# Optimization experiments

Measured on AMD Instinct MI355X. Metric: run time of the kernel, lower is better.

## Reference

```python
import jax, jax.numpy as jnp
import numpy as np

SIG_DEPTH = 4  # matches sig_depth init arg


def _outer(a, b):
    # flattened tensor product: [B, m] x [B, n] -> [B, m*n] (row-major, matches signatory layout)
    return (a[:, :, None] * b[:, None, :]).reshape(a.shape[0], -1)


def setup_inputs() -> dict:
    key = jax.random.key(0)
    k1, k2 = jax.random.split(key)
    B, L, Cin = 64, 256, 7
    out_dim = 512
    C = Cin + 1
    sig_channels = sum(C ** k for k in range(1, SIG_DEPTH + 1))  # 4680
    inp = jax.random.normal(k1, (B, L, Cin), dtype=jnp.float32)
    W = jax.random.normal(k2, (out_dim, sig_channels), dtype=jnp.float32) * 0.02
    b = jnp.zeros((out_dim,), dtype=jnp.float32)
    return {"inp": inp, "W": W, "b": b}


def reference(inp, W, b):
    B, L, Cin = inp.shape
    # Augment: prepend time channel linspace(0, 1, L), keep original channels
    t = jnp.broadcast_to(jnp.linspace(0.0, 1.0, L, dtype=inp.dtype)[None, :, None], (B, L, 1))
    x = jnp.concatenate([t, inp], axis=-1)  # [B, L, C]
    C = Cin + 1
    d = SIG_DEPTH
    dx = jnp.transpose(x[:, 1:] - x[:, :-1], (1, 0, 2))  # [L-1, B, C] increments
    init = tuple(jnp.zeros((B, C ** (k + 1)), x.dtype) for k in range(d))  # identity signature (all zero levels)

    def step(levels, v):
        # exp(v) in the truncated tensor algebra: e_k = v^{(x)k} / k!
        e = [v]
        for k in range(1, d):
            e.append(_outer(e[-1], v) / (k + 1))
        # Chen's identity: new_k = a_k + e_k + sum_{i=1}^{k-1} a_i (x) e_{k-i}
        new = []
        for k in range(d):
            acc = levels[k] + e[k]
            for i in range(k):
                acc = acc + _outer(levels[i], e[k - 1 - i])
            new.append(acc)
        sig = jnp.concatenate(new, axis=-1)  # [B, sig_channels]
        return tuple(new), sig

    _, sigs = jax.lax.scan(step, init, dx)  # [L-1, B, sig_channels] (stream=True)
    sigs = jnp.transpose(sigs, (1, 0, 2))   # [B, L-1, sig_channels]
    return sigs @ W.T + b                   # [B, L-1, out_dim]
```

## Files before the change

### kernel.cpp

```cpp
#include <hip/hip_runtime.h>
#include <hip/hip_bf16.h>

#define BATCH 64
#define LSEQ 256
#define CIN 7
#define CC 8
#define NSIG 4680
#define KPAD 4736
#define TSTEPS 255
#define ODIM 512
#define NCHUNK 16
#define CH 16
#define NKT 74
#define BM 256
#define BN 128

typedef __attribute__((ext_vector_type(8))) unsigned short ushort8;
typedef __attribute__((ext_vector_type(8))) __bf16 bf16x8;
typedef __attribute__((ext_vector_type(4))) float f32x4;

__device__ __forceinline__ unsigned short f2bf(float x) {
    __hip_bfloat16 h = __float2bfloat16(x);
    return *(unsigned short*)&h;
}

#define GLDS16(gp, lp)                                                      \
    __builtin_amdgcn_global_load_lds(                                       \
        (const __attribute__((address_space(1))) void*)(gp),                \
        (__attribute__((address_space(3))) void*)(lp), 16, 0, 0)

__global__ __launch_bounds__(512) void sig_ckpt_kernel(const float* __restrict__ inp,
                                                       float* __restrict__ ckpt) {
    __shared__ float sDx[TSTEPS * CC];

    const int b   = blockIdx.x;
    const int tid = threadIdx.x;

    const float* ip = inp + (size_t)b * LSEQ * CIN;
    for (int i = tid; i < TSTEPS * CC; i += 512) {
        int t = i >> 3, c = i & 7;
        sDx[i] = (c == 0) ? (1.0f / 255.0f)
                          : ip[(t + 1) * CIN + (c - 1)] - ip[t * CIN + (c - 1)];
    }
    __syncthreads();

    const int i1 = tid >> 6;
    const int i2 = (tid >> 3) & 7;
    const int i3 = tid & 7;

    float a1own = 0.0f, a2own = 0.0f, a3 = 0.0f;
    float a4[8];
#pragma unroll
    for (int e = 0; e < 8; ++e) a4[e] = 0.0f;

    for (int t = 0; t < 240; ++t) {
        const float* v = &sDx[t * CC];
        const float4 vlo = *(const float4*)&v[0];
        const float4 vhi = *(const float4*)&v[4];
        const float va = v[i1], vb = v[i2], vc = v[i3];
        const float e3s = va * vb * vc * (1.0f / 6.0f);
        const float T4 = e3s * 0.25f + a1own * vb * vc * (1.0f / 6.0f)
                       + a2own * vc * 0.5f + a3;
        a4[0] += vlo.x * T4; a4[1] += vlo.y * T4;
        a4[2] += vlo.z * T4; a4[3] += vlo.w * T4;
        a4[4] += vhi.x * T4; a4[5] += vhi.y * T4;
        a4[6] += vhi.z * T4; a4[7] += vhi.w * T4;
        a3 += e3s + (a1own * vb * 0.5f + a2own) * vc;
        a2own += vb * (0.5f * va + a1own);
        a1own += va;

        if (((t + 1) & 15) == 0) {
            const int c = ((t + 1) >> 4) - 1;
            float* cp = ckpt + ((size_t)b * 15 + c) * NSIG;
            if ((tid & 63) == 0) cp[i1] = a1own;
            if ((tid & 7) == 0) cp[8 + (tid >> 3)] = a2own;
            cp[72 + tid] = a3;
            float4 q0 = {a4[0], a4[1], a4[2], a4[3]};
            float4 q1 = {a4[4], a4[5], a4[6], a4[7]};
            *(float4*)&cp[584 + tid * 8]     = q0;
            *(float4*)&cp[584 + tid * 8 + 4] = q1;
        }
    }
}

__global__ __launch_bounds__(512) void sig_write_kernel(const float* __restrict__ inp,
                                                        const float* __restrict__ ckpt,
                                                        unsigned short* __restrict__ sig) {
    __shared__ float sDx[CH * CC];

    const int chunk = blockIdx.x;
    const int b     = blockIdx.y;
    const int tid   = threadIdx.x;
    const int t0    = chunk * CH;
    const int t1    = (chunk == NCHUNK - 1) ? TSTEPS : t0 + CH;

    const float* ip = inp + (size_t)b * LSEQ * CIN;
    for (int i = tid; i < (t1 - t0) * CC; i += 512) {
        int t = t0 + (i >> 3), c = i & 7;
        sDx[i] = (c == 0) ? (1.0f / 255.0f)
                          : ip[(t + 1) * CIN + (c - 1)] - ip[t * CIN + (c - 1)];
    }
    __syncthreads();

    const int i1 = tid >> 6;
    const int i2 = (tid >> 3) & 7;
    const int i3 = tid & 7;

    float a1own, a2own, a3;
    float a4[8];
    if (chunk == 0) {
        a1own = a2own = a3 = 0.0f;
#pragma unroll
        for (int e = 0; e < 8; ++e) a4[e] = 0.0f;
    } else {
        const float* cp = ckpt + ((size_t)b * 15 + (chunk - 1)) * NSIG;
        a1own = cp[i1];
        a2own = cp[8 + (tid >> 3)];
        a3    = cp[72 + tid];
        float4 q0 = *(const float4*)&cp[584 + tid * 8];
        float4 q1 = *(const float4*)&cp[584 + tid * 8 + 4];
        a4[0] = q0.x; a4[1] = q0.y; a4[2] = q0.z; a4[3] = q0.w;
        a4[4] = q1.x; a4[5] = q1.y; a4[6] = q1.z; a4[7] = q1.w;
    }

    for (int t = t0; t < t1; ++t) {
        const float* v = &sDx[(t - t0) * CC];
        const float4 vlo = *(const float4*)&v[0];
        const float4 vhi = *(const float4*)&v[4];
        const float va = v[i1], vb = v[i2], vc = v[i3];
        const float e3s = va * vb * vc * (1.0f / 6.0f);
        const float T4 = e3s * 0.25f + a1own * vb * vc * (1.0f / 6.0f)
                       + a2own * vc * 0.5f + a3;
        a4[0] += vlo.x * T4; a4[1] += vlo.y * T4;
        a4[2] += vlo.z * T4; a4[3] += vlo.w * T4;
        a4[4] += vhi.x * T4; a4[5] += vhi.y * T4;
        a4[6] += vhi.z * T4; a4[7] += vhi.w * T4;
        a3 += e3s + (a1own * vb * 0.5f + a2own) * vc;
        a2own += vb * (0.5f * va + a1own);
        a1own += va;

        unsigned short* row = sig + ((size_t)b * TSTEPS + t) * KPAD;
        ushort8 pack;
#pragma unroll
        for (int e = 0; e < 8; ++e) pack[e] = f2bf(a4[e]);
        *(ushort8*)(row + 584 + tid * 8) = pack;
        row[72 + tid] = f2bf(a3);
        if ((tid & 63) == 0) row[i1] = f2bf(a1own);
        if ((tid & 7) == 0) row[8 + (tid >> 3)] = f2bf(a2own);
        if (tid >= 448 && tid < 504) row[4232 + tid] = 0;
    }
}

__global__ __launch_bounds__(256) void wcvt_kernel(const float* __restrict__ W,
                                                   unsigned short* __restrict__ Wb) {
    int idx = blockIdx.x * 256 + threadIdx.x;
    if (idx >= ODIM * KPAD) return;
    int n = idx / KPAD, k = idx - n * KPAD;
    Wb[idx] = (k < NSIG) ? f2bf(W[(size_t)n * NSIG + k]) : (unsigned short)0;
}

__global__ __launch_bounds__(512) void gemm_kernel(const unsigned short* __restrict__ A,
                                                   const unsigned short* __restrict__ Wb,
                                                   const float* __restrict__ bias,
                                                   float* __restrict__ out,
                                                   int Mrows) {
    __shared__ unsigned short As[3][BM * 64];
    __shared__ unsigned short Bs[3][BN * 64];

    const int tid = threadIdx.x;
    int nt, mt;
    if (gridDim.y == 64) {
        const int li = blockIdx.y * 4 + blockIdx.x;
        const int x  = li & 7;
        const int j  = li >> 3;
        mt = x * 8 + (j >> 2);
        nt = j & 3;
    } else {
        nt = blockIdx.x; mt = blockIdx.y;
    }
    const int lane = tid & 63;
    const int wv   = tid >> 6;
    const int wr   = wv >> 1;
    const int wc   = wv & 1;
    const int lr   = lane & 15;
    const int lq   = lane >> 4;
    const int sb   = lr & 7;

    const f32x4 z4 = {0.0f, 0.0f, 0.0f, 0.0f};
    f32x4 acc[4][4];
#pragma unroll
    for (int i = 0; i < 4; ++i)
#pragma unroll
        for (int j = 0; j < 4; ++j) acc[i][j] = z4;

    const int srow = tid >> 3;
    const int gcb  = (tid & 7) ^ (srow & 7);
    const int scol = gcb * 8;

    const unsigned short* aptr[4];
    const unsigned short* bptr[2];
#pragma unroll
    for (int i = 0; i < 4; ++i) {
        int gr = mt * BM + i * 64 + srow;
        if (gr >= Mrows) gr = 0;
        aptr[i] = A + (size_t)gr * KPAD + scol;
    }
#pragma unroll
    for (int i = 0; i < 2; ++i)
        bptr[i] = Wb + (size_t)(nt * BN + i * 64 + srow) * KPAD + scol;

    const int kel0 = ((lq)     ^ sb) * 8;
    const int kel1 = ((4 + lq) ^ sb) * 8;

    const int aoff = (wr * 64 + lr) * 64;
    const int boff = (wc * 64 + lr) * 64;

#define STAGE_ALL(buf, koff)                                                \
    do {                                                                    \
        _Pragma("unroll")                                                   \
        for (int i_ = 0; i_ < 4; ++i_)                                      \
            GLDS16(aptr[i_] + (koff),                                       \
                   ((char*)As[buf]) + i_ * 8192 + tid * 16);                \
        _Pragma("unroll")                                                   \
        for (int i_ = 0; i_ < 2; ++i_)                                      \
            GLDS16(bptr[i_] + (koff),                                       \
                   ((char*)Bs[buf]) + i_ * 8192 + tid * 16);                \
    } while (0)

    STAGE_ALL(0, 0);
    STAGE_ALL(1, 64);
    asm volatile("s_waitcnt vmcnt(6)" ::: "memory");
    __builtin_amdgcn_sched_barrier(0);
    __builtin_amdgcn_s_barrier();
    __builtin_amdgcn_sched_barrier(0);

    int cur = 0, nxt = 1, nn = 2;
    for (int t = 0; t < NKT; ++t) {
        const unsigned short* as = &As[0][0] + cur * (BM * 64);
        const unsigned short* bs = &Bs[0][0] + cur * (BN * 64);
        const bool st = (t + 2 < NKT);
        const int koff = (t + 2) * 64;

        bf16x8 afP[4], bfP[4], afN[4], bfN[4];
#pragma unroll
        for (int i = 0; i < 4; ++i)
            afP[i] = *(const bf16x8*)&as[aoff + i * 1024 + kel0];
#pragma unroll
        for (int j = 0; j < 4; ++j)
            bfP[j] = *(const bf16x8*)&bs[boff + j * 1024 + kel0];
#pragma unroll
        for (int i = 0; i < 4; ++i)
            afN[i] = *(const bf16x8*)&as[aoff + i * 1024 + kel1];
#pragma unroll
        for (int j = 0; j < 4; ++j)
            bfN[j] = *(const bf16x8*)&bs[boff + j * 1024 + kel1];
        if (st) STAGE_ALL(nn, koff);

        asm volatile("s_waitcnt lgkmcnt(8)" ::: "memory");
        __builtin_amdgcn_sched_barrier(0);
        __builtin_amdgcn_s_setprio(1);
#pragma unroll
        for (int i = 0; i < 4; ++i)
#pragma unroll
            for (int j = 0; j < 4; ++j)
                acc[i][j] = __builtin_amdgcn_mfma_f32_16x16x32_bf16(
                    afP[i], bfP[j], acc[i][j], 0, 0, 0);
        __builtin_amdgcn_s_setprio(0);
        __builtin_amdgcn_sched_barrier(0);

        asm volatile("s_waitcnt lgkmcnt(0)" ::: "memory");
        __builtin_amdgcn_sched_barrier(0);
        __builtin_amdgcn_s_setprio(1);
#pragma unroll
        for (int i = 0; i < 4; ++i)
#pragma unroll
            for (int j = 0; j < 4; ++j)
                acc[i][j] = __builtin_amdgcn_mfma_f32_16x16x32_bf16(
                    afN[i], bfN[j], acc[i][j], 0, 0, 0);
        __builtin_amdgcn_s_setprio(0);
        __builtin_amdgcn_sched_barrier(0);

        if (st) {
            asm volatile("s_waitcnt vmcnt(6)" ::: "memory");
            __builtin_amdgcn_sched_barrier(0);
            __builtin_amdgcn_s_barrier();
            __builtin_amdgcn_sched_barrier(0);
        } else if (t + 1 < NKT) {
            asm volatile("s_waitcnt vmcnt(0)" ::: "memory");
            __builtin_amdgcn_sched_barrier(0);
            __builtin_amdgcn_s_barrier();
            __builtin_amdgcn_sched_barrier(0);
        }

        const int tmp = cur; cur = nxt; nxt = nn; nn = tmp;
    }

    float bn[4];
#pragma unroll
    for (int j = 0; j < 4; ++j)
        bn[j] = bias[nt * BN + wc * 64 + j * 16 + lr];

#pragma unroll
    for (int i = 0; i < 4; ++i) {
        const int mbase = mt * BM + wr * 64 + i * 16 + lq * 4;
#pragma unroll
        for (int r = 0; r < 4; ++r) {
            const int m = mbase + r;
            if (m < Mrows) {
#pragma unroll
                for (int j = 0; j < 4; ++j) {
                    const int n = nt * BN + wc * 64 + j * 16 + lr;
                    out[(size_t)m * ODIM + n] = acc[i][j][r] + bn[j];
                }
            }
        }
    }
#undef STAGE_ALL
}

extern "C" void kernel_launch(void* const* d_in, const int* in_sizes, int n_in,
                              void* d_out, int out_size, void* d_ws, size_t ws_size,
                              hipStream_t stream) {
    const float* inp  = (const float*)d_in[0];
    const float* W    = (const float*)d_in[1];
    const float* bias = (const float*)d_in[2];
    float* out = (float*)d_out;

    const size_t wbBytes = (size_t)ODIM * KPAD * sizeof(unsigned short);
    const size_t sigPB   = (size_t)TSTEPS * KPAD * sizeof(unsigned short);
    const size_t ckptPB  = (size_t)15 * NSIG * sizeof(float);
    const size_t perB    = sigPB + ckptPB;

    int nbMax = (int)((ws_size - wbBytes) / perB);
    if (nbMax > BATCH) nbMax = BATCH;
    if (nbMax < 1) nbMax = 1;

    unsigned short* sig  = (unsigned short*)d_ws;
    float*          ckpt = (float*)((char*)d_ws + (size_t)nbMax * sigPB);
    unsigned short* Wb   = (unsigned short*)((char*)d_ws + (ws_size - wbBytes));

    wcvt_kernel<<<(ODIM * KPAD + 255) / 256, 256, 0, stream>>>(W, Wb);

    for (int b0 = 0; b0 < BATCH; b0 += nbMax) {
        const int nb = (b0 + nbMax <= BATCH) ? nbMax : (BATCH - b0);
        const int Mrows = nb * TSTEPS;
        const float* ipb = inp + (size_t)b0 * LSEQ * CIN;
        sig_ckpt_kernel<<<nb, 512, 0, stream>>>(ipb, ckpt);
        sig_write_kernel<<<dim3(NCHUNK, nb), 512, 0, stream>>>(ipb, ckpt, sig);
        gemm_kernel<<<dim3(ODIM / BN, (Mrows + BM - 1) / BM), 512, 0, stream>>>(
            sig, Wb, bias, out + (size_t)b0 * TSTEPS * ODIM, Mrows);
    }
}
```

Baseline: 148.9 us.

## Merge weight conversion into checkpoint kernel, split checkpoint work, restructure GEMM pipeline

The checkpoint kernel now uses four blocks per batch element, each owning a quarter of the level-3 indices with two level-4 outputs per thread. It also absorbs the bf16 weight conversion as extra blocks that use vectorised 8-wide loads and stores, removing a separate launch and raising parallelism in the sequential scan. The GEMM main loop is rewritten as a fully unrolled triple-buffer schedule where the next tile's first-half fragments load after the barrier, overlapping with the second-half MFMAs. In exchange, each sDx load is redundantly repeated four times per batch element, and weight conversion is redone on every batch chunk when the workspace forces chunking.

```diff
diff --git a/kernel.cpp b/kernel.cpp
--- a/kernel.cpp
+++ b/kernel.cpp
@@ -14,6 +14,7 @@
 #define NKT 74
 #define BM 256
 #define BN 128
+#define WCVT_BLK 592
 
 typedef __attribute__((ext_vector_type(8))) unsigned short ushort8;
 typedef __attribute__((ext_vector_type(8))) __bf16 bf16x8;
@@ -29,56 +30,74 @@
         (const __attribute__((address_space(1))) void*)(gp),                \
         (__attribute__((address_space(3))) void*)(lp), 16, 0, 0)
 
-__global__ __launch_bounds__(512) void sig_ckpt_kernel(const float* __restrict__ inp,
-                                                       float* __restrict__ ckpt) {
+__global__ __launch_bounds__(512) void prep_kernel(const float* __restrict__ inp,
+                                                   float* __restrict__ ckpt,
+                                                   const float* __restrict__ W,
+                                                   unsigned short* __restrict__ Wb,
+                                                   int nb) {
     __shared__ float sDx[TSTEPS * CC];
-
-    const int b   = blockIdx.x;
+    const int bx  = blockIdx.x;
     const int tid = threadIdx.x;
 
-    const float* ip = inp + (size_t)b * LSEQ * CIN;
-    for (int i = tid; i < TSTEPS * CC; i += 512) {
-        int t = i >> 3, c = i & 7;
-        sDx[i] = (c == 0) ? (1.0f / 255.0f)
-                          : ip[(t + 1) * CIN + (c - 1)] - ip[t * CIN + (c - 1)];
-    }
-    __syncthreads();
-
-    const int i1 = tid >> 6;
-    const int i2 = (tid >> 3) & 7;
-    const int i3 = tid & 7;
-
-    float a1own = 0.0f, a2own = 0.0f, a3 = 0.0f;
-    float a4[8];
-#pragma unroll
-    for (int e = 0; e < 8; ++e) a4[e] = 0.0f;
-
-    for (int t = 0; t < 240; ++t) {
-        const float* v = &sDx[t * CC];
-        const float4 vlo = *(const float4*)&v[0];
-        const float4 vhi = *(const float4*)&v[4];
-        const float va = v[i1], vb = v[i2], vc = v[i3];
-        const float e3s = va * vb * vc * (1.0f / 6.0f);
-        const float T4 = e3s * 0.25f + a1own * vb * vc * (1.0f / 6.0f)
-                       + a2own * vc * 0.5f + a3;
-        a4[0] += vlo.x * T4; a4[1] += vlo.y * T4;
-        a4[2] += vlo.z * T4; a4[3] += vlo.w * T4;
-        a4[4] += vhi.x * T4; a4[5] += vhi.y * T4;
-        a4[6] += vhi.z * T4; a4[7] += vhi.w * T4;
-        a3 += e3s + (a1own * vb * 0.5f + a2own) * vc;
-        a2own += vb * (0.5f * va + a1own);
-        a1own += va;
-
-        if (((t + 1) & 15) == 0) {
-            const int c = ((t + 1) >> 4) - 1;
-            float* cp = ckpt + ((size_t)b * 15 + c) * NSIG;
-            if ((tid & 63) == 0) cp[i1] = a1own;
-            if ((tid & 7) == 0) cp[8 + (tid >> 3)] = a2own;
-            cp[72 + tid] = a3;
-            float4 q0 = {a4[0], a4[1], a4[2], a4[3]};
-            float4 q1 = {a4[4], a4[5], a4[6], a4[7]};
-            *(float4*)&cp[584 + tid * 8]     = q0;
-            *(float4*)&cp[584 + tid * 8 + 4] = q1;
+    if (bx < 4 * nb) {
+        const int b = bx >> 2, q = bx & 3;
+        const float* ip = inp + (size_t)b * LSEQ * CIN;
+        for (int i = tid; i < TSTEPS * CC; i += 512) {
+            int t = i >> 3, c = i & 7;
+            sDx[i] = (c == 0) ? (1.0f / 255.0f)
+                              : ip[(t + 1) * CIN + (c - 1)] - ip[t * CIN + (c - 1)];
+        }
+        __syncthreads();
+
+        const int o  = q * 128 + (tid >> 2);
+        const int e2 = tid & 3;
+        const int i1 = o >> 6, i2 = (o >> 3) & 7, i3 = o & 7;
+        float a1 = 0.0f, a2 = 0.0f, a3 = 0.0f, a4a = 0.0f, a4b = 0.0f;
+
+        for (int t = 0; t < 240; ++t) {
+            const float* v = &sDx[t * CC];
+            const float va = v[i1], vb = v[i2], vc = v[i3];
+            const float vA = v[e2], vB = v[e2 + 4];
+            const float e3s = va * vb * vc * (1.0f / 6.0f);
+            const float T4 = e3s * 0.25f + a1 * vb * vc * (1.0f / 6.0f)
+                           + a2 * vc * 0.5f + a3;
+            a4a += vA * T4;
+            a4b += vB * T4;
+            a3 += e3s + (a1 * vb * 0.5f + a2) * vc;
+            a2 += vb * (0.5f * va + a1);
+            a1 += va;
+
+            if (((t + 1) & 15) == 0) {
+                const int c = ((t + 1) >> 4) - 1;
+                float* cp = ckpt + ((size_t)b * 15 + c) * NSIG;
+                cp[584 + o * 8 + e2]     = a4a;
+                cp[584 + o * 8 + e2 + 4] = a4b;
+                if (e2 == 0) {
+                    cp[72 + o] = a3;
+                    if ((o & 7) == 0)  cp[8 + (o >> 3)] = a2;
+                    if ((o & 63) == 0) cp[i1] = a1;
+                }
+            }
+        }
+    } else {
+        const int vid = (bx - 4 * nb) * 512 + tid;
+        if (vid < ODIM * (KPAD / 8)) {
+            const int n = vid / (KPAD / 8);
+            const int g = vid - n * (KPAD / 8);
+            ushort8 pk;
+            if (g < NSIG / 8) {
+                const float* wp = W + (size_t)n * NSIG + g * 8;
+                float4 f0 = *(const float4*)wp;
+                float4 f1 = *(const float4*)(wp + 4);
+                pk[0] = f2bf(f0.x); pk[1] = f2bf(f0.y);
+                pk[2] = f2bf(f0.z); pk[3] = f2bf(f0.w);
+                pk[4] = f2bf(f1.x); pk[5] = f2bf(f1.y);
+                pk[6] = f2bf(f1.z); pk[7] = f2bf(f1.w);
+            } else {
+#pragma unroll
+                for (int e = 0; e < 8; ++e) pk[e] = 0;
+            }
+            *(ushort8*)(Wb + (size_t)n * KPAD + g * 8) = pk;
         }
     }
 }
@@ -151,14 +170,6 @@
     }
 }
 
-__global__ __launch_bounds__(256) void wcvt_kernel(const float* __restrict__ W,
-                                                   unsigned short* __restrict__ Wb) {
-    int idx = blockIdx.x * 256 + threadIdx.x;
-    if (idx >= ODIM * KPAD) return;
-    int n = idx / KPAD, k = idx - n * KPAD;
-    Wb[idx] = (k < NSIG) ? f2bf(W[(size_t)n * NSIG + k]) : (unsigned short)0;
-}
-
 __global__ __launch_bounds__(512) void gemm_kernel(const unsigned short* __restrict__ A,
                                                    const unsigned short* __restrict__ Wb,
                                                    const float* __restrict__ bias,
@@ -211,21 +222,39 @@
 
     const int kel0 = ((lq)     ^ sb) * 8;
     const int kel1 = ((4 + lq) ^ sb) * 8;
-
     const int aoff = (wr * 64 + lr) * 64;
     const int boff = (wc * 64 + lr) * 64;
 
-#define STAGE_ALL(buf, koff)                                                \
+#define STAGE_ALL(BUF, koff)                                                \
     do {                                                                    \
         _Pragma("unroll")                                                   \
         for (int i_ = 0; i_ < 4; ++i_)                                      \
             GLDS16(aptr[i_] + (koff),                                       \
-                   ((char*)As[buf]) + i_ * 8192 + tid * 16);                \
+                   ((char*)As[BUF]) + i_ * 8192 + tid * 16);                \
         _Pragma("unroll")                                                   \
         for (int i_ = 0; i_ < 2; ++i_)                                      \
             GLDS16(bptr[i_] + (koff),                                       \
-                   ((char*)Bs[buf]) + i_ * 8192 + tid * 16);                \
+                   ((char*)Bs[BUF]) + i_ * 8192 + tid * 16);                \
     } while (0)
+
+#define MFMA16(AF, BF)                                                      \
+    do {                                                                    \
+        _Pragma("unroll")                                                   \
+        for (int im_ = 0; im_ < 4; ++im_)                                   \
+            _Pragma("unroll")                                               \
+            for (int jm_ = 0; jm_ < 4; ++jm_)                               \
+                acc[im_][jm_] = __builtin_amdgcn_mfma_f32_16x16x32_bf16(    \
+                    AF[im_], BF[jm_], acc[im_][jm_], 0, 0, 0);              \
+    } while (0)
+
+#define LDF(DST, SRC, BASE, KEL)                                            \
+    do {                                                                    \
+        _Pragma("unroll")                                                   \
+        for (int l_ = 0; l_ < 4; ++l_)                                      \
+            DST[l_] = *(const bf16x8*)&SRC[(BASE) + l_ * 1024 + (KEL)];     \
+    } while (0)
+
+    bf16x8 afP[4], bfP[4], afN[4], bfN[4];
 
     STAGE_ALL(0, 0);
     STAGE_ALL(1, 64);
@@ -233,66 +262,86 @@
     __builtin_amdgcn_sched_barrier(0);
     __builtin_amdgcn_s_barrier();
     __builtin_amdgcn_sched_barrier(0);
-
-    int cur = 0, nxt = 1, nn = 2;
-    for (int t = 0; t < NKT; ++t) {
-        const unsigned short* as = &As[0][0] + cur * (BM * 64);
-        const unsigned short* bs = &Bs[0][0] + cur * (BN * 64);
-        const bool st = (t + 2 < NKT);
-        const int koff = (t + 2) * 64;
-
-        bf16x8 afP[4], bfP[4], afN[4], bfN[4];
-#pragma unroll
-        for (int i = 0; i < 4; ++i)
-            afP[i] = *(const bf16x8*)&as[aoff + i * 1024 + kel0];
-#pragma unroll
-        for (int j = 0; j < 4; ++j)
-            bfP[j] = *(const bf16x8*)&bs[boff + j * 1024 + kel0];
-#pragma unroll
-        for (int i = 0; i < 4; ++i)
-            afN[i] = *(const bf16x8*)&as[aoff + i * 1024 + kel1];
-#pragma unroll
-        for (int j = 0; j < 4; ++j)
-            bfN[j] = *(const bf16x8*)&bs[boff + j * 1024 + kel1];
-        if (st) STAGE_ALL(nn, koff);
-
+    LDF(afP, (&As[0][0]), aoff, kel0);
+    LDF(bfP, (&Bs[0][0]), boff, kel0);
+    __builtin_amdgcn_sched_barrier(0);
+
+    int koff = 128;
+
+#define TILE_FULL(CUR, NXT, NN)                                             \
+    {                                                                       \
+        LDF(afN, (&As[CUR][0]), aoff, kel1);                                \
+        LDF(bfN, (&Bs[CUR][0]), boff, kel1);                                \
+        STAGE_ALL(NN, koff);                                                \
+        koff += 64;                                                         \
+        __builtin_amdgcn_sched_barrier(0);                                  \
+        asm volatile("s_waitcnt lgkmcnt(8)" ::: "memory");                  \
+        __builtin_amdgcn_sched_barrier(0);                                  \
+        __builtin_amdgcn_s_setprio(1);                                      \
+        MFMA16(afP, bfP);                                                   \
+        __builtin_amdgcn_s_setprio(0);                                      \
+        __builtin_amdgcn_sched_barrier(0);                                  \
+        asm volatile("s_waitcnt lgkmcnt(0)" ::: "memory");                  \
+        __builtin_amdgcn_sched_barrier(0);                                  \
+        asm volatile("s_waitcnt vmcnt(6)" ::: "memory");                    \
+        __builtin_amdgcn_sched_barrier(0);                                  \
+        __builtin_amdgcn_s_barrier();                                       \
+        __builtin_amdgcn_sched_barrier(0);                                  \
+        LDF(afP, (&As[NXT][0]), aoff, kel0);                                \
+        LDF(bfP, (&Bs[NXT][0]), boff, kel0);                                \
+        __builtin_amdgcn_sched_barrier(0);                                  \
+        __builtin_amdgcn_s_setprio(1);                                      \
+        MFMA16(afN, bfN);                                                   \
+        __builtin_amdgcn_s_setprio(0);                                      \
+        __builtin_amdgcn_sched_barrier(0);                                  \
+    }
+
+    for (int tb = 0; tb < 24; ++tb) {
+        TILE_FULL(0, 1, 2);
+        TILE_FULL(1, 2, 0);
+        TILE_FULL(2, 0, 1);
+    }
+
+    {
+        LDF(afN, (&As[0][0]), aoff, kel1);
+        LDF(bfN, (&Bs[0][0]), boff, kel1);
+        __builtin_amdgcn_sched_barrier(0);
         asm volatile("s_waitcnt lgkmcnt(8)" ::: "memory");
         __builtin_amdgcn_sched_barrier(0);
         __builtin_amdgcn_s_setprio(1);
-#pragma unroll
-        for (int i = 0; i < 4; ++i)
-#pragma unroll
-            for (int j = 0; j < 4; ++j)
-                acc[i][j] = __builtin_amdgcn_mfma_f32_16x16x32_bf16(
-                    afP[i], bfP[j], acc[i][j], 0, 0, 0);
+        MFMA16(afP, bfP);
         __builtin_amdgcn_s_setprio(0);
         __builtin_amdgcn_sched_barrier(0);
-
         asm volatile("s_waitcnt lgkmcnt(0)" ::: "memory");
         __builtin_amdgcn_sched_barrier(0);
+        asm volatile("s_waitcnt vmcnt(0)" ::: "memory");
+        __builtin_amdgcn_sched_barrier(0);
+        __builtin_amdgcn_s_barrier();
+        __builtin_amdgcn_sched_barrier(0);
+        LDF(afP, (&As[1][0]), aoff, kel0);
+        LDF(bfP, (&Bs[1][0]), boff, kel0);
+        __builtin_amdgcn_sched_barrier(0);
         __builtin_amdgcn_s_setprio(1);
-#pragma unroll
-        for (int i = 0; i < 4; ++i)
-#pragma unroll
-            for (int j = 0; j < 4; ++j)
-                acc[i][j] = __builtin_amdgcn_mfma_f32_16x16x32_bf16(
-                    afN[i], bfN[j], acc[i][j], 0, 0, 0);
+        MFMA16(afN, bfN);
         __builtin_amdgcn_s_setprio(0);
         __builtin_amdgcn_sched_barrier(0);
-
-        if (st) {
-            asm volatile("s_waitcnt vmcnt(6)" ::: "memory");
-            __builtin_amdgcn_sched_barrier(0);
-            __builtin_amdgcn_s_barrier();
-            __builtin_amdgcn_sched_barrier(0);
-        } else if (t + 1 < NKT) {
-            asm volatile("s_waitcnt vmcnt(0)" ::: "memory");
-            __builtin_amdgcn_sched_barrier(0);
-            __builtin_amdgcn_s_barrier();
-            __builtin_amdgcn_sched_barrier(0);
-        }
-
-        const int tmp = cur; cur = nxt; nxt = nn; nn = tmp;
+    }
+    {
+        LDF(afN, (&As[1][0]), aoff, kel1);
+        LDF(bfN, (&Bs[1][0]), boff, kel1);
+        __builtin_amdgcn_sched_barrier(0);
+        asm volatile("s_waitcnt lgkmcnt(8)" ::: "memory");
+        __builtin_amdgcn_sched_barrier(0);
+        __builtin_amdgcn_s_setprio(1);
+        MFMA16(afP, bfP);
+        __builtin_amdgcn_s_setprio(0);
+        __builtin_amdgcn_sched_barrier(0);
+        asm volatile("s_waitcnt lgkmcnt(0)" ::: "memory");
+        __builtin_amdgcn_sched_barrier(0);
+        __builtin_amdgcn_s_setprio(1);
+        MFMA16(afN, bfN);
+        __builtin_amdgcn_s_setprio(0);
+        __builtin_amdgcn_sched_barrier(0);
     }
 
     float bn[4];
@@ -316,6 +365,9 @@
         }
     }
 #undef STAGE_ALL
+#undef MFMA16
+#undef LDF
+#undef TILE_FULL
 }
 
 extern "C" void kernel_launch(void* const* d_in, const int* in_sizes, int n_in,
@@ -339,13 +391,11 @@
     float*          ckpt = (float*)((char*)d_ws + (size_t)nbMax * sigPB);
     unsigned short* Wb   = (unsigned short*)((char*)d_ws + (ws_size - wbBytes));
 
-    wcvt_kernel<<<(ODIM * KPAD + 255) / 256, 256, 0, stream>>>(W, Wb);
-
     for (int b0 = 0; b0 < BATCH; b0 += nbMax) {
         const int nb = (b0 + nbMax <= BATCH) ? nbMax : (BATCH - b0);
         const int Mrows = nb * TSTEPS;
         const float* ipb = inp + (size_t)b0 * LSEQ * CIN;
-        sig_ckpt_kernel<<<nb, 512, 0, stream>>>(ipb, ckpt);
+        prep_kernel<<<4 * nb + WCVT_BLK, 512, 0, stream>>>(ipb, ckpt, W, Wb, nb);
         sig_write_kernel<<<dim3(NCHUNK, nb), 512, 0, stream>>>(ipb, ckpt, sig);
         gemm_kernel<<<dim3(ODIM / BN, (Mrows + BM - 1) / BM), 512, 0, stream>>>(
             sig, Wb, bias, out + (size_t)b0 * TSTEPS * ODIM, Mrows);
```

New measurement: 147.7 us. No clear change (-0.8%).
